# Kernel optimization log

Hardware: AMD Instinct MI355X
Metric: run time of the kernel (lower is better)

The kernel has to match this reference:

```python
import jax, jax.numpy as jnp
import numpy as np


def setup_inputs() -> dict:
    key = jax.random.key(0)
    k1, k2 = jax.random.split(key)
    B, K, D = 65536, 4096, 64
    x = jax.random.normal(k1, (B, D), dtype=jnp.float32)
    nodes = jax.random.normal(k2, (K, D), dtype=jnp.float32)  # self.nodes parameter
    return {"x": x, "nodes": nodes}


def reference(x, nodes):
    # torch.cdist(x, nodes, p=2): Euclidean distance matrix [B, K]
    x2 = jnp.sum(x * x, axis=-1, keepdims=True)            # [B, 1]
    n2 = jnp.sum(nodes * nodes, axis=-1)[None, :]          # [1, K]
    d2 = x2 + n2 - 2.0 * (x @ nodes.T)                     # [B, K]
    distances = jnp.sqrt(jnp.maximum(d2, 0.0))
    winning_indices = jnp.argmin(distances, axis=-1)       # [B]
    node_repr = nodes[winning_indices]                     # [B, D] gather
    return node_repr, winning_indices
```

## Files before the change

### kernel.cpp

```cpp
#include <hip/hip_runtime.h>
#include <stdint.h>


typedef unsigned short u16;
typedef __bf16 bf16x8 __attribute__((ext_vector_type(8)));
typedef unsigned short u16x8 __attribute__((ext_vector_type(8)));
typedef float f32x16 __attribute__((ext_vector_type(16)));

#define B_ROWS 65536
#define K_NODES 4096
#define DIM 64
#define MERGE_TAU 0.0065f

#define SN 128
#define HSTAGES 16

#define OFF_LIST 64
#define OFF_N2F  262208
#define OFF_N2D  278592
#define OFF_BFRAG 311360

#define GLOBAL_AS __attribute__((address_space(1)))
#define LDS_AS    __attribute__((address_space(3)))

__device__ __forceinline__ u16 bf16_rne(float f, float& back) {
    uint32_t u = __float_as_uint(f);
    uint32_t r = u + 0x7FFFu + ((u >> 16) & 1u);
    u16 h = (u16)(r >> 16);
    back = __uint_as_float(((uint32_t)h) << 16);
    return h;
}

__device__ __forceinline__ float pack_tile6(float v, uint32_t t) {
    return __uint_as_float((__float_as_uint(v) & 0xFFFFFFC0u) | t);
}

__global__ __launch_bounds__(256) void prep(const float* __restrict__ nodes,
                                            u16* __restrict__ bfrag,
                                            float* __restrict__ hn2f,
                                            double* __restrict__ n2d,
                                            int* __restrict__ ref_cnt) {
    if (blockIdx.x < 128) {
        int idx = blockIdx.x * 256 + threadIdx.x;
        int t = idx >> 8;
        int rem = idx & 255;
        int l = rem >> 2, c = rem & 3;
        const float* row = nodes + (size_t)(t * 32 + (l & 31)) * DIM + ((l >> 5) * 8);
        float4 f0 = *(const float4*)(row + c * 16);
        float4 f1 = *(const float4*)(row + c * 16 + 4);
        float fs[8] = {-f0.x, -f0.y, -f0.z, -f0.w, -f1.x, -f1.y, -f1.z, -f1.w};
        u16x8 hv, lv;
        #pragma unroll
        for (int j = 0; j < 8; ++j) {
            float hf, dummy;
            u16 hb = bf16_rne(fs[j], hf);
            u16 lb = bf16_rne(fs[j] - hf, dummy);
            hv[j] = hb; lv[j] = lb;
        }
        int base = ((t * 4 + c) * 2) * 512 + l * 8;
        *(u16x8*)(bfrag + base)       = hv;
        *(u16x8*)(bfrag + base + 512) = lv;
    } else {
        if (blockIdx.x == 128 && threadIdx.x == 0) *ref_cnt = 0;
        int k = (blockIdx.x - 128) * 256 + threadIdx.x;
        if (k < K_NODES) {
            const float* r = nodes + (size_t)k * DIM;
            double s = 0.0;
            #pragma unroll
            for (int d = 0; d < DIM; ++d) { double v = (double)r[d]; s += v * v; }
            n2d[k] = s;
            hn2f[k] = 0.5f * (float)s;
        }
    }
}

__global__ __launch_bounds__(256, 2) void phase1(const float* __restrict__ x,
                                                 const u16* __restrict__ bfrag_g,
                                                 const float* __restrict__ hn2f,
                                                 float* __restrict__ out) {
    __shared__ __align__(16) u16 sb[2][16384];
    const int tid  = threadIdx.x;
    const int lane = tid & 63;
    const int w    = tid >> 6;
    const int col  = lane & 31;
    const int lh   = lane >> 5;
    const int rb   = blockIdx.x >> 1;
    const int h    = blockIdx.x & 1;
    const int rbase = rb * 256 + w * 64;

    bf16x8 ah[2][4], al[2][4];
    #pragma unroll
    for (int t = 0; t < 2; ++t) {
        const float* xp = x + (size_t)(rbase + t * 32 + col) * DIM + lh * 8;
        #pragma unroll
        for (int c = 0; c < 4; ++c) {
            float4 f0 = *(const float4*)(xp + c * 16);
            float4 f1 = *(const float4*)(xp + c * 16 + 4);
            float fs[8] = {f0.x, f0.y, f0.z, f0.w, f1.x, f1.y, f1.z, f1.w};
            u16x8 hv, lv;
            #pragma unroll
            for (int j = 0; j < 8; ++j) {
                float hf, dummy;
                u16 hb = bf16_rne(fs[j], hf);
                u16 lb = bf16_rne(fs[j] - hf, dummy);
                hv[j] = hb; lv[j] = lb;
            }
            union { u16x8 u; bf16x8 b; } cvh, cvl;
            cvh.u = hv; cvl.u = lv;
            ah[t][c] = cvh.b; al[t][c] = cvl.b;
        }
    }

    float b1[2][16], v2[2][16];
    #pragma unroll
    for (int t = 0; t < 2; ++t)
        #pragma unroll
        for (int q = 0; q < 16; ++q) { b1[t][q] = 3.4e38f; v2[t][q] = 3.4e38f; }

    const char* gbase = (const char*)bfrag_g;
    const float* hp = hn2f + col;
    const int s0g = h * HSTAGES;

    {
        const char* gp = gbase + (size_t)s0g * 32768 + tid * 16;
        const char* lp = (const char*)&sb[0][0] + tid * 16;
        #pragma unroll
        for (int i = 0; i < 8; ++i)
            __builtin_amdgcn_global_load_lds(
                (const GLOBAL_AS uint32_t*)(gp + i * 4096),
                (LDS_AS uint32_t*)(lp + i * 4096), 16, 0, 0);
    }
    __syncthreads();

    int cur = 0;
    for (int sl = 0; sl < HSTAGES; ++sl) {
        const int s = s0g + sl;
        if (sl + 1 < HSTAGES) {
            const char* gp = gbase + (size_t)(s + 1) * 32768 + tid * 16;
            const char* lp = (const char*)&sb[cur ^ 1][0] + tid * 16;
            #pragma unroll
            for (int i = 0; i < 8; ++i)
                __builtin_amdgcn_global_load_lds(
                    (const GLOBAL_AS uint32_t*)(gp + i * 4096),
                    (LDS_AS uint32_t*)(lp + i * 4096), 16, 0, 0);
        }

        float hn2v[4];
        #pragma unroll
        for (int nt = 0; nt < 4; ++nt) hn2v[nt] = hp[s * SN + nt * 32];

        const u16* bb = &sb[cur][0];
        #pragma unroll
        for (int nt = 0; nt < 4; ++nt) {
            f32x16 a0, a1;
            #pragma unroll
            for (int q = 0; q < 16; ++q) { a0[q] = hn2v[nt]; a1[q] = hn2v[nt]; }
            #pragma unroll
            for (int c = 0; c < 4; ++c) {
                const bf16x8 bh = *(const bf16x8*)(bb + ((nt * 4 + c) * 2 + 0) * 512 + lane * 8);
                const bf16x8 bl = *(const bf16x8*)(bb + ((nt * 4 + c) * 2 + 1) * 512 + lane * 8);
                a0 = __builtin_amdgcn_mfma_f32_32x32x16_bf16(ah[0][c], bh, a0, 0, 0, 0);
                a1 = __builtin_amdgcn_mfma_f32_32x32x16_bf16(ah[1][c], bh, a1, 0, 0, 0);
                a0 = __builtin_amdgcn_mfma_f32_32x32x16_bf16(al[0][c], bh, a0, 0, 0, 0);
                a1 = __builtin_amdgcn_mfma_f32_32x32x16_bf16(al[1][c], bh, a1, 0, 0, 0);
                a0 = __builtin_amdgcn_mfma_f32_32x32x16_bf16(ah[0][c], bl, a0, 0, 0, 0);
                a1 = __builtin_amdgcn_mfma_f32_32x32x16_bf16(ah[1][c], bl, a1, 0, 0, 0);
            }
            const uint32_t tb = (uint32_t)(sl * 4 + nt);
            #pragma unroll
            for (int q = 0; q < 16; ++q) {
                float p0 = pack_tile6(a0[q], tb);
                v2[0][q] = fminf(v2[0][q], fmaxf(p0, b1[0][q]));
                b1[0][q] = fminf(b1[0][q], p0);
                float p1 = pack_tile6(a1[q], tb);
                v2[1][q] = fminf(v2[1][q], fmaxf(p1, b1[1][q]));
                b1[1][q] = fminf(b1[1][q], p1);
            }
        }

        __syncthreads();
        cur ^= 1;
    }

    int gi[2][16];
    #pragma unroll
    for (int t = 0; t < 2; ++t)
        #pragma unroll
        for (int q = 0; q < 16; ++q)
            gi[t][q] = h * 2048 + (int)(__float_as_uint(b1[t][q]) & 63u) * 32 + col;

    #pragma unroll
    for (int off = 1; off < 32; off <<= 1) {
        #pragma unroll
        for (int t = 0; t < 2; ++t)
            #pragma unroll
            for (int q = 0; q < 16; ++q) {
                float ov  = __shfl_xor(b1[t][q], off, 64);
                float ov2 = __shfl_xor(v2[t][q], off, 64);
                int   og  = __shfl_xor(gi[t][q], off, 64);
                float hi2 = fmaxf(b1[t][q], ov);
                v2[t][q] = fminf(fminf(v2[t][q], ov2), hi2);
                bool take = (ov < b1[t][q]) || (ov == b1[t][q] && og < gi[t][q]);
                b1[t][q] = take ? ov : b1[t][q];
                gi[t][q] = take ? og : gi[t][q];
            }
    }

    if (col == 0) {
        #pragma unroll
        for (int t = 0; t < 2; ++t)
            #pragma unroll
            for (int q = 0; q < 16; ++q) {
                int rloc = (q & 3) + 8 * (q >> 2) + 4 * lh;
                int grow = rb * 256 + w * 64 + t * 32 + rloc;
                *(float2*)(out + (size_t)grow * DIM + h * 2) = make_float2(b1[t][q], v2[t][q]);
                out[(size_t)grow * DIM + 4 + h] = (float)gi[t][q];
            }
    }
}

__global__ __launch_bounds__(256) void merge_k(const float* __restrict__ nodes,
                                               float* __restrict__ out,
                                               int* __restrict__ ref_cnt,
                                               int* __restrict__ ref_list) {
    __shared__ int s_win[256];
    const int tid = threadIdx.x;
    const int row = blockIdx.x * 256 + tid;
    float4 cv = *(const float4*)(out + (size_t)row * DIM);
    float2 ci = *(const float2*)(out + (size_t)row * DIM + 4);
    bool h1w = cv.z < cv.x;
    float wb  = h1w ? cv.z : cv.x;
    float lb  = h1w ? cv.x : cv.z;
    float v2m = fminf(fminf(cv.y, cv.w), lb);
    int gi = (int)(h1w ? ci.y : ci.x);
    out[(size_t)B_ROWS * DIM + row] = (float)gi;
    if (v2m - wb <= MERGE_TAU) {
        int slot = atomicAdd(ref_cnt, 1);
        ref_list[slot] = row;
    }
    s_win[tid] = gi;
    __syncthreads();
    const int base_row = blockIdx.x * 256;
    for (int i = tid; i < 256 * 16; i += 256) {
        int rr = i >> 4, cc = i & 15;
        int wn = s_win[rr];
        float4 v = *(const float4*)(nodes + (size_t)wn * DIM + cc * 4);
        *(float4*)(out + (size_t)(base_row + rr) * DIM + cc * 4) = v;
    }
}

__global__ __launch_bounds__(256) void phase2(const float* __restrict__ x,
                                              const float* __restrict__ nodes,
                                              const double* __restrict__ n2d,
                                              const int* __restrict__ ref_cnt,
                                              const int* __restrict__ ref_list,
                                              float* __restrict__ out) {
    __shared__ double xsA[DIM], xsB[DIM];
    __shared__ double sval[256];
    __shared__ int    sidx[256];
    __shared__ int    rows_s[2];
    const int tid = threadIdx.x;
    const int cnt = *ref_cnt;
    for (int b0 = blockIdx.x * 2; b0 < cnt; b0 += gridDim.x * 2) {
        const int nr = min(2, cnt - b0);
        __syncthreads();
        if (tid < 2) rows_s[tid] = ref_list[b0 + min(tid, nr - 1)];
        __syncthreads();
        if (tid < DIM) {
            xsA[tid] = (double)x[(size_t)rows_s[0] * DIM + tid];
            xsB[tid] = (double)x[(size_t)rows_s[1] * DIM + tid];
        }
        __syncthreads();

        double bestA = 1e300, bestB = 1e300;
        int    biA = K_NODES, biB = K_NODES;
        for (int k = tid; k < K_NODES; k += 256) {
            const float4* np4 = (const float4*)(nodes + (size_t)k * DIM);
            double a0 = 0.0, a1 = 0.0, b0d = 0.0, b1d = 0.0;
            #pragma unroll
            for (int t = 0; t < 16; t += 2) {
                float4 w0 = np4[t], w1 = np4[t + 1];
                a0 += xsA[t*4+0]*(double)w0.x + xsA[t*4+1]*(double)w0.y
                    + xsA[t*4+2]*(double)w0.z + xsA[t*4+3]*(double)w0.w;
                b0d += xsB[t*4+0]*(double)w0.x + xsB[t*4+1]*(double)w0.y
                     + xsB[t*4+2]*(double)w0.z + xsB[t*4+3]*(double)w0.w;
                a1 += xsA[t*4+4]*(double)w1.x + xsA[t*4+5]*(double)w1.y
                    + xsA[t*4+6]*(double)w1.z + xsA[t*4+7]*(double)w1.w;
                b1d += xsB[t*4+4]*(double)w1.x + xsB[t*4+5]*(double)w1.y
                     + xsB[t*4+6]*(double)w1.z + xsB[t*4+7]*(double)w1.w;
            }
            const double nn = n2d[k];
            double sA = nn - 2.0 * (a0 + a1);
            double sB = nn - 2.0 * (b0d + b1d);
            if (sA < bestA) { bestA = sA; biA = k; }
            if (sB < bestB) { bestB = sB; biB = k; }
        }

        #pragma unroll 1
        for (int r = 0; r < nr; ++r) {
            sval[tid] = (r == 0) ? bestA : bestB;
            sidx[tid] = (r == 0) ? biA : biB;
            __syncthreads();
            for (int stride = 128; stride > 0; stride >>= 1) {
                if (tid < (unsigned)stride) {
                    double ov = sval[tid + stride];
                    int    oi = sidx[tid + stride];
                    if (ov < sval[tid] || (ov == sval[tid] && oi < sidx[tid])) {
                        sval[tid] = ov; sidx[tid] = oi;
                    }
                }
                __syncthreads();
            }
            const int wn = sidx[0];
            const int row = rows_s[r];
            if (tid == 0) out[(size_t)B_ROWS * DIM + row] = (float)wn;
            if (tid < 16) {
                float4 v = *(const float4*)(nodes + (size_t)wn * DIM + tid * 4);
                *(float4*)(out + (size_t)row * DIM + tid * 4) = v;
            }
            __syncthreads();
        }
    }
}

extern "C" void kernel_launch(void* const* d_in, const int* in_sizes, int n_in,
                              void* d_out, int out_size, void* d_ws, size_t ws_size,
                              hipStream_t stream) {
    const float* x     = (const float*)d_in[0];
    const float* nodes = (const float*)d_in[1];
    float* out = (float*)d_out;
    char*  ws  = (char*)d_ws;

    int*    ref_cnt  = (int*)ws;
    int*    ref_list = (int*)(ws + OFF_LIST);
    float*  hn2f     = (float*)(ws + OFF_N2F);
    double* n2d      = (double*)(ws + OFF_N2D);
    u16*    bfrag    = (u16*)(ws + OFF_BFRAG);

    prep<<<144, 256, 0, stream>>>(nodes, bfrag, hn2f, n2d, ref_cnt);
    phase1<<<512, 256, 0, stream>>>(x, bfrag, hn2f, out);
    merge_k<<<B_ROWS / 256, 256, 0, stream>>>(nodes, out, ref_cnt, ref_list);
    phase2<<<1024, 256, 0, stream>>>(x, nodes, n2d, ref_cnt, ref_list, out);
}
```

Baseline: 170.7 us.

## Replace double-buffered stage loop with 8-slot LDS ring and finer-grained prefetch

```diff
diff --git a/kernel.cpp b/kernel.cpp
--- a/kernel.cpp
+++ b/kernel.cpp
@@ -11,9 +11,6 @@
 #define K_NODES 4096
 #define DIM 64
 #define MERGE_TAU 0.0065f
-
-#define SN 128
-#define HSTAGES 16
 
 #define OFF_LIST 64
 #define OFF_N2F  262208
@@ -78,7 +75,8 @@
                                                  const u16* __restrict__ bfrag_g,
                                                  const float* __restrict__ hn2f,
                                                  float* __restrict__ out) {
-    __shared__ __align__(16) u16 sb[2][16384];
+    __shared__ __align__(16) u16 ring[32768];
+    __shared__ float hn2s[2048];
     const int tid  = threadIdx.x;
     const int lane = tid & 63;
     const int w    = tid >> 6;
@@ -87,6 +85,7 @@
     const int rb   = blockIdx.x >> 1;
     const int h    = blockIdx.x & 1;
     const int rbase = rb * 256 + w * 64;
+    const char* qbase = (const char*)bfrag_g + (size_t)h * 524288;
 
     bf16x8 ah[2][4], al[2][4];
     #pragma unroll
@@ -117,70 +116,79 @@
         #pragma unroll
         for (int q = 0; q < 16; ++q) { b1[t][q] = 3.4e38f; v2[t][q] = 3.4e38f; }
 
-    const char* gbase = (const char*)bfrag_g;
-    const float* hp = hn2f + col;
-    const int s0g = h * HSTAGES;
-
-    {
-        const char* gp = gbase + (size_t)s0g * 32768 + tid * 16;
-        const char* lp = (const char*)&sb[0][0] + tid * 16;
-        #pragma unroll
-        for (int i = 0; i < 8; ++i)
-            __builtin_amdgcn_global_load_lds(
-                (const GLOBAL_AS uint32_t*)(gp + i * 4096),
-                (LDS_AS uint32_t*)(lp + i * 4096), 16, 0, 0);
-    }
-    __syncthreads();
-
-    int cur = 0;
-    for (int sl = 0; sl < HSTAGES; ++sl) {
-        const int s = s0g + sl;
-        if (sl + 1 < HSTAGES) {
-            const char* gp = gbase + (size_t)(s + 1) * 32768 + tid * 16;
-            const char* lp = (const char*)&sb[cur ^ 1][0] + tid * 16;
-            #pragma unroll
-            for (int i = 0; i < 8; ++i)
-                __builtin_amdgcn_global_load_lds(
-                    (const GLOBAL_AS uint32_t*)(gp + i * 4096),
-                    (LDS_AS uint32_t*)(lp + i * 4096), 16, 0, 0);
-        }
-
-        float hn2v[4];
-        #pragma unroll
-        for (int nt = 0; nt < 4; ++nt) hn2v[nt] = hp[s * SN + nt * 32];
-
-        const u16* bb = &sb[cur][0];
-        #pragma unroll
-        for (int nt = 0; nt < 4; ++nt) {
-            f32x16 a0, a1;
-            #pragma unroll
-            for (int q = 0; q < 16; ++q) { a0[q] = hn2v[nt]; a1[q] = hn2v[nt]; }
-            #pragma unroll
-            for (int c = 0; c < 4; ++c) {
-                const bf16x8 bh = *(const bf16x8*)(bb + ((nt * 4 + c) * 2 + 0) * 512 + lane * 8);
-                const bf16x8 bl = *(const bf16x8*)(bb + ((nt * 4 + c) * 2 + 1) * 512 + lane * 8);
-                a0 = __builtin_amdgcn_mfma_f32_32x32x16_bf16(ah[0][c], bh, a0, 0, 0, 0);
-                a1 = __builtin_amdgcn_mfma_f32_32x32x16_bf16(ah[1][c], bh, a1, 0, 0, 0);
-                a0 = __builtin_amdgcn_mfma_f32_32x32x16_bf16(al[0][c], bh, a0, 0, 0, 0);
-                a1 = __builtin_amdgcn_mfma_f32_32x32x16_bf16(al[1][c], bh, a1, 0, 0, 0);
-                a0 = __builtin_amdgcn_mfma_f32_32x32x16_bf16(ah[0][c], bl, a0, 0, 0, 0);
-                a1 = __builtin_amdgcn_mfma_f32_32x32x16_bf16(ah[1][c], bl, a1, 0, 0, 0);
-            }
-            const uint32_t tb = (uint32_t)(sl * 4 + nt);
-            #pragma unroll
-            for (int q = 0; q < 16; ++q) {
-                float p0 = pack_tile6(a0[q], tb);
-                v2[0][q] = fminf(v2[0][q], fmaxf(p0, b1[0][q]));
-                b1[0][q] = fminf(b1[0][q], p0);
-                float p1 = pack_tile6(a1[q], tb);
-                v2[1][q] = fminf(v2[1][q], fmaxf(p1, b1[1][q]));
-                b1[1][q] = fminf(b1[1][q], p1);
-            }
-        }
-
-        __syncthreads();
-        cur ^= 1;
-    }
+    for (int i = tid; i < 2048; i += 256) hn2s[i] = hn2f[h * 2048 + i];
+    #pragma unroll
+    for (int q0 = 0; q0 < 4; ++q0) {
+        const char* gp = qbase + (size_t)q0 * 8192 + tid * 16;
+        const char* lp = (const char*)ring + q0 * 8192 + tid * 16;
+        __builtin_amdgcn_global_load_lds((const GLOBAL_AS uint32_t*)gp,
+                                         (LDS_AS uint32_t*)lp, 16, 0, 0);
+        __builtin_amdgcn_global_load_lds((const GLOBAL_AS uint32_t*)(gp + 4096),
+                                         (LDS_AS uint32_t*)(lp + 4096), 16, 0, 0);
+    }
+    asm volatile("s_waitcnt lgkmcnt(0)" ::: "memory");
+    __builtin_amdgcn_s_barrier();
+
+#define MF6(CC, BH, BL)                                                          \
+    a0 = __builtin_amdgcn_mfma_f32_32x32x16_bf16(ah[0][CC], BH, a0, 0, 0, 0);    \
+    a1 = __builtin_amdgcn_mfma_f32_32x32x16_bf16(ah[1][CC], BH, a1, 0, 0, 0);    \
+    a0 = __builtin_amdgcn_mfma_f32_32x32x16_bf16(al[0][CC], BH, a0, 0, 0, 0);    \
+    a1 = __builtin_amdgcn_mfma_f32_32x32x16_bf16(al[1][CC], BH, a1, 0, 0, 0);    \
+    a0 = __builtin_amdgcn_mfma_f32_32x32x16_bf16(ah[0][CC], BL, a0, 0, 0, 0);    \
+    a1 = __builtin_amdgcn_mfma_f32_32x32x16_bf16(ah[1][CC], BL, a1, 0, 0, 0);
+
+#define PHASE(QI, VMSTR) do {                                                    \
+    asm volatile("s_waitcnt " VMSTR ::: "memory");                               \
+    __builtin_amdgcn_s_barrier();                                                \
+    __builtin_amdgcn_sched_barrier(0);                                           \
+    const u16* bb = ring + ((QI) & 7) * 4096;                                    \
+    bf16x8 B0h = *(const bf16x8*)(bb + 0 * 1024 + lane * 8);                     \
+    bf16x8 B0l = *(const bf16x8*)(bb + 0 * 1024 + 512 + lane * 8);               \
+    bf16x8 B1h = *(const bf16x8*)(bb + 1 * 1024 + lane * 8);                     \
+    bf16x8 B1l = *(const bf16x8*)(bb + 1 * 1024 + 512 + lane * 8);               \
+    bf16x8 B2h = *(const bf16x8*)(bb + 2 * 1024 + lane * 8);                     \
+    bf16x8 B2l = *(const bf16x8*)(bb + 2 * 1024 + 512 + lane * 8);               \
+    bf16x8 B3h = *(const bf16x8*)(bb + 3 * 1024 + lane * 8);                     \
+    bf16x8 B3l = *(const bf16x8*)(bb + 3 * 1024 + 512 + lane * 8);               \
+    float hn2v = hn2s[(QI) * 32 + col];                                          \
+    if ((QI) + 4 < 64) {                                                         \
+        const char* gp = qbase + (size_t)((QI) + 4) * 8192 + tid * 16;           \
+        const char* lp = (const char*)ring + (((QI) + 4) & 7) * 8192 + tid * 16; \
+        __builtin_amdgcn_global_load_lds((const GLOBAL_AS uint32_t*)gp,          \
+                                         (LDS_AS uint32_t*)lp, 16, 0, 0);        \
+        __builtin_amdgcn_global_load_lds((const GLOBAL_AS uint32_t*)(gp + 4096), \
+                                         (LDS_AS uint32_t*)(lp + 4096), 16, 0, 0); \
+    }                                                                            \
+    asm volatile("s_waitcnt lgkmcnt(0)" ::: "memory");                           \
+    __builtin_amdgcn_sched_barrier(0);                                           \
+    f32x16 a0, a1;                                                               \
+    _Pragma("unroll")                                                            \
+    for (int q = 0; q < 16; ++q) { a0[q] = hn2v; a1[q] = hn2v; }                 \
+    __builtin_amdgcn_s_setprio(1);                                               \
+    MF6(0, B0h, B0l)                                                             \
+    MF6(1, B1h, B1l)                                                             \
+    MF6(2, B2h, B2l)                                                             \
+    MF6(3, B3h, B3l)                                                             \
+    __builtin_amdgcn_s_setprio(0);                                               \
+    const uint32_t tb = (uint32_t)(QI);                                          \
+    _Pragma("unroll")                                                            \
+    for (int q = 0; q < 16; ++q) {                                               \
+        float p0 = pack_tile6(a0[q], tb);                                        \
+        v2[0][q] = fminf(v2[0][q], fmaxf(p0, b1[0][q]));                         \
+        b1[0][q] = fminf(b1[0][q], p0);                                          \
+        float p1 = pack_tile6(a1[q], tb);                                        \
+        v2[1][q] = fminf(v2[1][q], fmaxf(p1, b1[1][q]));                         \
+        b1[1][q] = fminf(b1[1][q], p1);                                          \
+    }                                                                            \
+} while (0)
+
+    for (int qi = 0; qi < 61; ++qi) PHASE(qi, "vmcnt(6)");
+    PHASE(61, "vmcnt(4)");
+    PHASE(62, "vmcnt(2)");
+    PHASE(63, "vmcnt(0)");
+
+#undef PHASE
+#undef MF6
 
     int gi[2][16];
     #pragma unroll
```

Result: slower. 182.4 us (+6.8%).
